# Optimization experiments

Hardware: AMD Instinct MI355X
Metric: run time of the kernel (lower is better)

The kernel has to match this reference:

```python
import jax, jax.numpy as jnp
import numpy as np


def setup_inputs() -> dict:
    key = jax.random.key(0)
    ks = jax.random.split(key, 8)
    B, D, H, W = 4, 96, 64, 64
    K, N, R = 4, 16, 6
    return {
        "x": jax.random.normal(ks[0], (B, D, H, W), jnp.float32),
        "x_proj_weight": jax.random.normal(ks[1], (K, R + 2 * N, D), jnp.float32) * 0.05,
        "dt_projs_weight": jax.random.normal(ks[2], (K, D, R), jnp.float32) * 0.1,
        "dt_projs_bias": jax.random.normal(ks[3], (K, D), jnp.float32) * 0.1,
        "A_logs": jax.random.uniform(ks[4], (K * D, N), jnp.float32),
        "Ds": jax.random.normal(ks[5], (K * D,), jnp.float32),
        "ln_weight": jnp.ones((D,), jnp.float32),
        "ln_bias": jnp.zeros((D,), jnp.float32),
    }


def reference(x, x_proj_weight, dt_projs_weight, dt_projs_bias, A_logs, Ds, ln_weight, ln_bias):
    B, D, H, W = x.shape
    K, _, R = dt_projs_weight.shape
    N = A_logs.shape[1]
    L = H * W

    # ---- CrossScan: 4 traversal orders (row-major, col-major, and their reverses) ----
    xf = x.reshape(B, D, L)                                   # row-major
    xt = jnp.transpose(x, (0, 1, 3, 2)).reshape(B, D, L)      # col-major
    xs = jnp.stack([xf, xt, xf[..., ::-1], xt[..., ::-1]], axis=1)  # (B, K, D, L)

    # ---- input-dependent projections ----
    x_dbl = jnp.einsum('bkdl,kcd->bkcl', xs, x_proj_weight)   # (B, K, R+2N, L)
    dts, Bs, Cs = jnp.split(x_dbl, [R, R + N], axis=2)        # Bs/Cs: (B, K, N, L)
    dts = jnp.einsum('bkrl,kdr->bkdl', dts, dt_projs_weight)  # (B, K, D, L)

    A = -jnp.exp(A_logs).reshape(K, D, N)                     # (K, D, N)
    delta = jax.nn.softplus(dts + dt_projs_bias[None, :, :, None])  # (B, K, D, L)

    # ---- selective (S6) scan over L ----
    def step(h, inp):
        d_t, u_t, B_t, C_t = inp  # (B,K,D) (B,K,D) (B,K,N) (B,K,N)
        dA = jnp.exp(d_t[..., None] * A[None])                # (B,K,D,N)
        h = h * dA + (d_t * u_t)[..., None] * B_t[:, :, None, :]
        y_t = jnp.einsum('bkdn,bkn->bkd', h, C_t)
        return h, y_t

    h0 = jnp.zeros((B, K, D, N), x.dtype)
    seq = (jnp.moveaxis(delta, -1, 0), jnp.moveaxis(xs, -1, 0),
           jnp.moveaxis(Bs, -1, 0), jnp.moveaxis(Cs, -1, 0))
    _, ys = jax.lax.scan(step, h0, seq)                       # (L, B, K, D)
    ys = jnp.moveaxis(ys, 0, -1)                              # (B, K, D, L)
    ys = ys + Ds.reshape(K, D)[None, :, :, None] * xs         # skip term D*u

    # ---- CrossMerge: undo the 4 traversal orders and sum ----
    m = ys[:, 0:2] + ys[:, 2:4][..., ::-1]                    # (B, 2, D, L)
    y = m[:, 0] + jnp.transpose(m[:, 1].reshape(B, D, W, H), (0, 1, 3, 2)).reshape(B, D, L)

    # ---- out_norm (LayerNorm over channels, v0 path) ----
    y = jnp.transpose(y, (0, 2, 1))                           # (B, L, D)
    mu = y.mean(-1, keepdims=True)
    var = y.var(-1, keepdims=True)
    y = (y - mu) / jnp.sqrt(var + 1e-5) * ln_weight + ln_bias
    return y.reshape(B, H, W, D)
```

## Files before the change

### kernel.cpp

```cpp
#include <hip/hip_runtime.h>
#include <math.h>

#define B_ 4
#define D_ 96
#define H_ 64
#define W_ 64
#define L_ 4096
#define K_ 4
#define N_ 16
#define R_ 6
#define C_ 38
#define SSX 128
#define CLSX (L_ / SSX)
#define CH_ (B_ * K_ * D_ * N_)

#if defined(__has_builtin)
#if __has_builtin(__builtin_amdgcn_exp2f)
#define EXP2F(x) __builtin_amdgcn_exp2f(x)
#else
#define EXP2F(x) exp2f(x)
#endif
#else
#define EXP2F(x) exp2f(x)
#endif
#define LOG2E 1.44269504f

__device__ __forceinline__ int src_idx(int k, int l) {
    int m = (k >= 2) ? (L_ - 1 - l) : l;
    if (k & 1) return ((m & 63) << 6) | (m >> 6);
    return m;
}

__device__ __forceinline__ float softplus_f(float a) {
    return (a > 15.f) ? a : __logf(1.f + __expf(a));
}

__global__ __launch_bounds__(256) void transpose_kernel(
    const float* __restrict__ x,
    float* __restrict__ xs2)
{
    int bid = blockIdx.x;
    int b = bid / (3 * 64);
    int rest = bid % (3 * 64);
    int dblk = rest / 64, lblk = rest % 64;
    int d0 = dblk * 32;
    int l0 = lblk * 64;
    int tid = threadIdx.x;

    __shared__ float s_t[32][65];

    for (int i = tid; i < 32 * 64; i += 256) {
        int d = i >> 6, l = i & 63;
        s_t[d][l] = x[((long)b * D_ + d0 + d) * L_ + l0 + l];
    }
    __syncthreads();

    for (int i = tid; i < 64 * 32; i += 256) {
        int l = i >> 5, d = i & 31;
        float v = s_t[d][l];
        xs2[((long)b * L_ + l0 + l) * D_ + d0 + d] = v;
        xs2[((long)(B_ + b) * L_ + l * 64 + lblk) * D_ + d0 + d] = v;
    }
}

__global__ __launch_bounds__(256) void proj_kernel(
    const float* __restrict__ xs2,
    const float* __restrict__ xpw,
    const float* __restrict__ wdt,
    const float* __restrict__ bdt,
    float* __restrict__ delta,
    float* __restrict__ Bsb,
    float* __restrict__ Csb)
{
    const int TL = 64;
    const int tiles = L_ / TL;
    int bid = blockIdx.x;
    int bk = bid / tiles;
    int tile = bid % tiles;
    int b = bk / K_, k = bk % K_;
    int l0 = tile * TL;
    int tid = threadIdx.x;

    __shared__ __align__(16) float s_wpT[D_ * 40];
    __shared__ __align__(16) float s_xs[D_ * 68];
    __shared__ __align__(16) float s_wdt[R_ * D_];
    __shared__ __align__(16) float s_bias[D_];
    __shared__ __align__(16) float s_dts[R_ * 68];

    for (int i = tid; i < C_ * D_; i += 256) {
        int d = i / C_, c = i % C_;
        int cp = (c < 6) ? c : c + 2;
        s_wpT[d * 40 + cp] = xpw[(k * C_ + c) * D_ + d];
    }
    for (int i = tid; i < 96; i += 256) {
        s_wpT[i * 40 + 6] = 0.f;
        s_wpT[i * 40 + 7] = 0.f;
    }
    for (int i = tid; i < R_ * D_; i += 256) {
        int r = i / D_, d = i % D_;
        s_wdt[i] = wdt[(k * D_ + d) * R_ + r];
    }
    if (tid < D_) s_bias[tid] = bdt[k * D_ + tid];

    const float* xsp = xs2 + (long)((k & 1) * B_ + b) * L_ * D_;
    for (int i = tid; i < TL * 24; i += 256) {
        int lt = i / 24, dq = i % 24;
        int row = (k < 2) ? (l0 + lt) : (L_ - 1 - l0 - lt);
        float4 v = *(const float4*)(xsp + (long)row * D_ + dq * 4);
        s_xs[(dq * 4 + 0) * 68 + lt] = v.x;
        s_xs[(dq * 4 + 1) * 68 + lt] = v.y;
        s_xs[(dq * 4 + 2) * 68 + lt] = v.z;
        s_xs[(dq * 4 + 3) * 68 + lt] = v.w;
    }
    __syncthreads();

    long base = (long)bk * L_ + l0;

    int ct = tid >> 4;
    int lt4 = (tid & 15) * 4;
    if (ct < 10) {
        int cp0 = ct * 4;
        float acc[4][4];
#pragma unroll
        for (int i = 0; i < 4; ++i)
#pragma unroll
            for (int j = 0; j < 4; ++j) acc[i][j] = 0.f;
#pragma unroll 4
        for (int d = 0; d < D_; ++d) {
            float4 wv = *(const float4*)(&s_wpT[d * 40 + cp0]);
            float4 xv = *(const float4*)(&s_xs[d * 68 + lt4]);
            float wa[4] = {wv.x, wv.y, wv.z, wv.w};
            float xa[4] = {xv.x, xv.y, xv.z, xv.w};
#pragma unroll
            for (int ci = 0; ci < 4; ++ci)
#pragma unroll
                for (int li = 0; li < 4; ++li)
                    acc[ci][li] += wa[ci] * xa[li];
        }
        if (ct == 0) {
#pragma unroll
            for (int ci = 0; ci < 4; ++ci)
                *(float4*)(&s_dts[ci * 68 + lt4]) =
                    make_float4(acc[ci][0], acc[ci][1], acc[ci][2], acc[ci][3]);
        } else if (ct == 1) {
#pragma unroll
            for (int ci = 0; ci < 2; ++ci)
                *(float4*)(&s_dts[(4 + ci) * 68 + lt4]) =
                    make_float4(acc[ci][0], acc[ci][1], acc[ci][2], acc[ci][3]);
        } else if (ct < 6) {
            int n0 = cp0 - 8;
#pragma unroll
            for (int li = 0; li < 4; ++li)
                *(float4*)(&Bsb[(base + lt4 + li) * N_ + n0]) =
                    make_float4(acc[0][li], acc[1][li], acc[2][li], acc[3][li]);
        } else {
            int n0 = cp0 - 24;
#pragma unroll
            for (int li = 0; li < 4; ++li)
                *(float4*)(&Csb[(base + lt4 + li) * N_ + n0]) =
                    make_float4(acc[0][li], acc[1][li], acc[2][li], acc[3][li]);
        }
    }
    __syncthreads();

    for (int tt = tid; tt < 24 * 16; tt += 256) {
        int dt = tt % 24, lt4b = (tt / 24) * 4;
        int d0 = dt * 4;
        float4 bias = *(const float4*)(&s_bias[d0]);
        float acc[4][4];
#pragma unroll
        for (int li = 0; li < 4; ++li) {
            acc[li][0] = bias.x; acc[li][1] = bias.y;
            acc[li][2] = bias.z; acc[li][3] = bias.w;
        }
#pragma unroll
        for (int r = 0; r < R_; ++r) {
            float4 wv = *(const float4*)(&s_wdt[r * D_ + d0]);
            float4 tv = *(const float4*)(&s_dts[r * 68 + lt4b]);
            float wa[4] = {wv.x, wv.y, wv.z, wv.w};
            float ta[4] = {tv.x, tv.y, tv.z, tv.w};
#pragma unroll
            for (int li = 0; li < 4; ++li)
#pragma unroll
                for (int di = 0; di < 4; ++di)
                    acc[li][di] += ta[li] * wa[di];
        }
#pragma unroll
        for (int li = 0; li < 4; ++li) {
            float4 o = make_float4(softplus_f(acc[li][0]), softplus_f(acc[li][1]),
                                   softplus_f(acc[li][2]), softplus_f(acc[li][3]));
            *(float4*)(&delta[(base + lt4b + li) * D_ + d0]) = o;
        }
    }
}

__global__ __launch_bounds__(384) void scan_part1(
    const float* __restrict__ A_logs,
    const float* __restrict__ xs2,
    const float* __restrict__ delta,
    const float* __restrict__ Bsb,
    float* __restrict__ pAarr,
    float* __restrict__ hharr)
{
    int tid = threadIdx.x;
    int sub = tid / 192;
    int r = tid % 192;
    int dd = r >> 1;
    int half = r & 1;
    int n0 = half * 8;
    int cid = blockIdx.x * 2 + sub;
    int bk = cid / SSX;
    int j = cid % SSX;
    int b = bk / K_, k = bk % K_;
    int kd = k * D_ + dd;
    int l0 = j * CLSX;

    float A2[8];
    {
        const float4* ap = (const float4*)(A_logs + kd * N_ + n0);
        float4 a0 = ap[0], a1 = ap[1];
        A2[0] = -__expf(a0.x) * LOG2E; A2[1] = -__expf(a0.y) * LOG2E;
        A2[2] = -__expf(a0.z) * LOG2E; A2[3] = -__expf(a0.w) * LOG2E;
        A2[4] = -__expf(a1.x) * LOG2E; A2[5] = -__expf(a1.y) * LOG2E;
        A2[6] = -__expf(a1.z) * LOG2E; A2[7] = -__expf(a1.w) * LOG2E;
    }

    const float* dp = delta + ((long)bk * L_ + l0) * D_ + dd;
    const float* bp = Bsb + ((long)bk * L_ + l0) * N_ + n0;
    const float* xsp = xs2 + (long)((k & 1) * B_ + b) * L_ * D_;
    long urow0 = (k < 2) ? l0 : (L_ - 1 - l0);
    long ustep = (k < 2) ? D_ : -D_;
    const float* up = xsp + urow0 * D_ + dd;

    float h[8];
#pragma unroll
    for (int i = 0; i < 8; ++i) h[i] = 0.f;
    float sdel = 0.f;

#pragma unroll 4
    for (int t = 0; t < CLSX; ++t) {
        float del = dp[(long)t * D_];
        float u   = up[(long)t * ustep];
        float4 b0 = *(const float4*)(bp + t * N_);
        float4 b1 = *(const float4*)(bp + t * N_ + 4);
        float Bv[8] = {b0.x, b0.y, b0.z, b0.w, b1.x, b1.y, b1.z, b1.w};
        sdel += del;
        float delu = del * u;
#pragma unroll
        for (int i = 0; i < 8; ++i) {
            float dA = EXP2F(del * A2[i]);
            h[i] = h[i] * dA + delu * Bv[i];
        }
    }

    long sbase = (long)j * CH_ + (long)(bk * D_ + dd) * N_ + n0;
    *(float4*)(pAarr + sbase) =
        make_float4(EXP2F(A2[0] * sdel), EXP2F(A2[1] * sdel),
                    EXP2F(A2[2] * sdel), EXP2F(A2[3] * sdel));
    *(float4*)(pAarr + sbase + 4) =
        make_float4(EXP2F(A2[4] * sdel), EXP2F(A2[5] * sdel),
                    EXP2F(A2[6] * sdel), EXP2F(A2[7] * sdel));
    *(float4*)(hharr + sbase)     = make_float4(h[0], h[1], h[2], h[3]);
    *(float4*)(hharr + sbase + 4) = make_float4(h[4], h[5], h[6], h[7]);
}

__global__ __launch_bounds__(256) void scan_combine(
    const float* __restrict__ pAarr,
    float* __restrict__ hharr)
{
    int c = blockIdx.x * 256 + threadIdx.x;
    float h = 0.f;
#pragma unroll 8
    for (int j = 0; j < SSX; ++j) {
        long idx = (long)j * CH_ + c;
        float tmp = hharr[idx];
        float pa  = pAarr[idx];
        hharr[idx] = h;
        h = tmp + pa * h;
    }
}

__global__ __launch_bounds__(384) void scan_part2_pair(
    const float* __restrict__ A_logs,
    const float* __restrict__ Ds,
    const float* __restrict__ xs2,
    const float* __restrict__ delta,
    const float* __restrict__ Bsb,
    const float* __restrict__ Csb,
    const float* __restrict__ hharr,
    float* __restrict__ ypair)
{
    __shared__ float s_y[2][CLSX][D_];

    int bid = blockIdx.x;
    int b = bid / (2 * SSX);
    int rest = bid % (2 * SSX);
    int p = rest / SSX;
    int j = rest % SSX;
    int tid = threadIdx.x;
    int g = tid / 192;
    int r = tid % 192;
    int dd = r >> 1;
    int half = r & 1;
    int n0 = half * 8;

    int kdir = p + 2 * g;
    int bk = b * K_ + kdir;
    int jj = g ? (SSX - 1 - j) : j;
    int l0s = jj * CLSX;
    int kd = kdir * D_ + dd;

    float A2[8];
    {
        const float4* ap = (const float4*)(A_logs + kd * N_ + n0);
        float4 a0 = ap[0], a1 = ap[1];
        A2[0] = -__expf(a0.x) * LOG2E; A2[1] = -__expf(a0.y) * LOG2E;
        A2[2] = -__expf(a0.z) * LOG2E; A2[3] = -__expf(a0.w) * LOG2E;
        A2[4] = -__expf(a1.x) * LOG2E; A2[5] = -__expf(a1.y) * LOG2E;
        A2[6] = -__expf(a1.z) * LOG2E; A2[7] = -__expf(a1.w) * LOG2E;
    }
    float Dv = Ds[kd];

    const float* dp = delta + ((long)bk * L_ + l0s) * D_ + dd;
    const float* bp = Bsb + ((long)bk * L_ + l0s) * N_ + n0;
    const float* cp = Csb + ((long)bk * L_ + l0s) * N_ + n0;
    const float* xsp = xs2 + (long)(p * B_ + b) * L_ * D_;
    long urow0 = g ? ((long)j * CLSX + CLSX - 1) : (long)l0s;
    long ustep = g ? -D_ : D_;
    const float* up = xsp + urow0 * D_ + dd;

    float h[8];
    {
        long sbase = (long)jj * CH_ + (long)(bk * D_ + dd) * N_ + n0;
        float4 h0 = *(const float4*)(hharr + sbase);
        float4 h1 = *(const float4*)(hharr + sbase + 4);
        h[0] = h0.x; h[1] = h0.y; h[2] = h0.z; h[3] = h0.w;
        h[4] = h1.x; h[5] = h1.y; h[6] = h1.z; h[7] = h1.w;
    }

#pragma unroll 4
    for (int t = 0; t < CLSX; ++t) {
        float del = dp[(long)t * D_];
        float u   = up[(long)t * ustep];
        float4 b0 = *(const float4*)(bp + t * N_);
        float4 b1 = *(const float4*)(bp + t * N_ + 4);
        float4 c0 = *(const float4*)(cp + t * N_);
        float4 c1 = *(const float4*)(cp + t * N_ + 4);
        float Bv[8] = {b0.x, b0.y, b0.z, b0.w, b1.x, b1.y, b1.z, b1.w};
        float Cv[8] = {c0.x, c0.y, c0.z, c0.w, c1.x, c1.y, c1.z, c1.w};
        float delu = del * u;
        float yv = 0.f;
#pragma unroll
        for (int i = 0; i < 8; ++i) {
            float dA = EXP2F(del * A2[i]);
            h[i] = h[i] * dA + delu * Bv[i];
            yv += h[i] * Cv[i];
        }
        yv += __shfl_xor(yv, 1);
        if (half == 0) {
            int tpos = g ? (CLSX - 1 - t) : t;
            s_y[g][tpos][dd] = yv + Dv * u;
        }
    }
    __syncthreads();

    float* yo = ypair + ((long)(p * B_ + b) * L_ + (long)j * CLSX) * D_;
    for (int i = tid; i < CLSX * 24; i += 384) {
        int lt = i / 24, dq = i % 24;
        int d0 = dq * 4;
        float4 o = make_float4(s_y[0][lt][d0 + 0] + s_y[1][lt][d0 + 0],
                               s_y[0][lt][d0 + 1] + s_y[1][lt][d0 + 1],
                               s_y[0][lt][d0 + 2] + s_y[1][lt][d0 + 2],
                               s_y[0][lt][d0 + 3] + s_y[1][lt][d0 + 3]);
        *(float4*)(yo + (long)lt * D_ + d0) = o;
    }
}

__global__ __launch_bounds__(256) void ln_merge_kernel(
    const float* __restrict__ ypair,
    const float* __restrict__ lnw,
    const float* __restrict__ lnb,
    float* __restrict__ out)
{
    int wid = (blockIdx.x * 256 + threadIdx.x) >> 6;
    int lane = threadIdx.x & 63;
    int b = wid / L_;
    int m = wid % L_;
    int mt = ((m & 63) << 6) | (m >> 6);

    const float* y0 = ypair + ((long)b * L_ + m) * D_;
    const float* y1 = ypair + ((long)(B_ + b) * L_ + mt) * D_;

    float v0 = y0[lane] + y1[lane];
    float v1 = (lane < 32) ? (y0[64 + lane] + y1[64 + lane]) : 0.f;

    float s  = v0 + v1;
    float s2 = v0 * v0 + v1 * v1;
#pragma unroll
    for (int mm = 1; mm < 64; mm <<= 1) {
        s  += __shfl_xor(s, mm);
        s2 += __shfl_xor(s2, mm);
    }
    float mu  = s * (1.f / D_);
    float var = s2 * (1.f / D_) - mu * mu;
    float rstd = rsqrtf(var + 1e-5f);

    long obase = (long)wid * D_;
    out[obase + lane] = (v0 - mu) * rstd * lnw[lane] + lnb[lane];
    if (lane < 32)
        out[obase + 64 + lane] = (v1 - mu) * rstd * lnw[64 + lane] + lnb[64 + lane];
}

__global__ __launch_bounds__(256) void proj_legacy(
    const float* __restrict__ x,
    const float* __restrict__ xpw,
    const float* __restrict__ wdt,
    const float* __restrict__ bdt,
    float* __restrict__ delta,
    float* __restrict__ Bsb,
    float* __restrict__ Csb)
{
    const int TL = 64;
    const int tiles = L_ / TL;
    int bid = blockIdx.x;
    int bk = bid / tiles;
    int tile = bid % tiles;
    int b = bk / K_, k = bk % K_;
    int l0 = tile * TL;
    int tid = threadIdx.x;

    __shared__ float s_wp[C_ * D_];
    __shared__ float s_wdt[R_ * D_];
    __shared__ float s_bias[D_];
    __shared__ float s_xs[D_ * (TL + 1)];
    __shared__ float s_xdbl[C_ * (TL + 1)];

    for (int i = tid; i < C_ * D_; i += 256) s_wp[i] = xpw[k * C_ * D_ + i];
    for (int i = tid; i < R_ * D_; i += 256) {
        int r = i / D_, d = i % D_;
        s_wdt[i] = wdt[(k * D_ + d) * R_ + r];
    }
    if (tid < D_) s_bias[tid] = bdt[k * D_ + tid];
    for (int i = tid; i < D_ * TL; i += 256) {
        int d = i / TL, lt = i % TL;
        s_xs[d * (TL + 1) + lt] = x[(b * D_ + d) * L_ + src_idx(k, l0 + lt)];
    }
    __syncthreads();

    for (int idx = tid; idx < C_ * TL; idx += 256) {
        int c = idx / TL, lt = idx % TL;
        const float* wr = &s_wp[c * D_];
        float acc = 0.f;
#pragma unroll 8
        for (int d = 0; d < D_; ++d) acc += wr[d] * s_xs[d * (TL + 1) + lt];
        s_xdbl[c * (TL + 1) + lt] = acc;
    }
    __syncthreads();

    long base = (long)bk * L_ + l0;
    for (int idx = tid; idx < TL * D_; idx += 256) {
        int lt = idx / D_, d = idx % D_;
        float acc = s_bias[d];
#pragma unroll
        for (int r = 0; r < R_; ++r)
            acc += s_wdt[r * D_ + d] * s_xdbl[r * (TL + 1) + lt];
        delta[(base + lt) * D_ + d] = softplus_f(acc);
    }
    for (int idx = tid; idx < TL * 2 * N_; idx += 256) {
        int lt = idx / (2 * N_), c2 = idx % (2 * N_);
        float v = s_xdbl[(R_ + c2) * (TL + 1) + lt];
        if (c2 < N_) Bsb[(base + lt) * N_ + c2] = v;
        else         Csb[(base + lt) * N_ + (c2 - N_)] = v;
    }
}

__global__ __launch_bounds__(64) void scan_serial(
    const float* __restrict__ x,
    const float* __restrict__ A_logs,
    const float* __restrict__ Ds,
    const float* __restrict__ delta,
    const float* __restrict__ Bsb,
    const float* __restrict__ Csb,
    float* __restrict__ ys)
{
    const int chans = D_ / 4;
    int bid = blockIdx.x;
    int bk = bid / chans;
    int d0 = (bid % chans) * 4;
    int b = bk / K_, k = bk % K_;
    int lane = threadIdx.x;
    int g = lane >> 4, n = lane & 15;
    int d = d0 + g;
    int kd = k * D_ + d;

    float A  = -__expf(A_logs[kd * N_ + n]);
    float Dv = Ds[kd];
    const float* dptr = delta + ((long)bk * L_) * D_ + d;
    const float* bptr = Bsb + (long)bk * L_ * N_ + n;
    const float* cptr = Csb + (long)bk * L_ * N_ + n;
    const float* xptr = x + ((long)b * D_ + d) * L_;
    float* yptr = ys + ((long)bk * L_) * D_ + d;

    float h = 0.f;
#pragma unroll 4
    for (int l = 0; l < L_; ++l) {
        float del = dptr[(long)l * D_];
        float u   = xptr[src_idx(k, l)];
        float Bt  = bptr[l * N_];
        float Ct  = cptr[l * N_];
        float dA  = __expf(del * A);
        h = h * dA + del * u * Bt;
        float yv = h * Ct;
        yv += __shfl_xor(yv, 1);
        yv += __shfl_xor(yv, 2);
        yv += __shfl_xor(yv, 4);
        yv += __shfl_xor(yv, 8);
        if (n == 0) yptr[(long)l * D_] = yv + Dv * u;
    }
}

__global__ __launch_bounds__(256) void merge_ln_kernel(
    const float* __restrict__ ys,
    const float* __restrict__ lnw,
    const float* __restrict__ lnb,
    float* __restrict__ out)
{
    int wid = (blockIdx.x * 256 + threadIdx.x) >> 6;
    int lane = threadIdx.x & 63;
    int b = wid / L_;
    int l = wid % L_;
    int lt = ((l & 63) << 6) | (l >> 6);

    long base0 = ((long)(b * K_ + 0) * L_ + l) * D_;
    long base2 = ((long)(b * K_ + 2) * L_ + (L_ - 1 - l)) * D_;
    long base1 = ((long)(b * K_ + 1) * L_ + lt) * D_;
    long base3 = ((long)(b * K_ + 3) * L_ + (L_ - 1 - lt)) * D_;

    int dA = lane;
    int dB = lane + 64;
    float v0 = ys[base0 + dA] + ys[base2 + dA] + ys[base1 + dA] + ys[base3 + dA];
    float v1 = 0.f;
    if (dB < D_)
        v1 = ys[base0 + dB] + ys[base2 + dB] + ys[base1 + dB] + ys[base3 + dB];

    float s  = v0 + v1;
    float s2 = v0 * v0 + v1 * v1;
#pragma unroll
    for (int m = 1; m < 64; m <<= 1) {
        s  += __shfl_xor(s, m);
        s2 += __shfl_xor(s2, m);
    }
    float mu  = s * (1.f / D_);
    float var = s2 * (1.f / D_) - mu * mu;
    float rstd = rsqrtf(var + 1e-5f);

    long obase = ((long)b * L_ + l) * D_;
    out[obase + dA] = (v0 - mu) * rstd * lnw[dA] + lnb[dA];
    if (dB < D_)
        out[obase + dB] = (v1 - mu) * rstd * lnw[dB] + lnb[dB];
}

extern "C" void kernel_launch(void* const* d_in, const int* in_sizes, int n_in,
                              void* d_out, int out_size, void* d_ws, size_t ws_size,
                              hipStream_t stream) {
    const float* x      = (const float*)d_in[0];
    const float* xpw    = (const float*)d_in[1];
    const float* wdt    = (const float*)d_in[2];
    const float* bdt    = (const float*)d_in[3];
    const float* A_logs = (const float*)d_in[4];
    const float* Ds     = (const float*)d_in[5];
    const float* lnw    = (const float*)d_in[6];
    const float* lnb    = (const float*)d_in[7];
    float* out = (float*)d_out;

    float* ws = (float*)d_ws;
    const long n_delta = (long)B_ * K_ * L_ * D_;
    const long n_bc    = (long)B_ * K_ * L_ * N_;
    const long n_bld   = (long)B_ * L_ * D_;
    const long n_sum   = (long)SSX * CH_;

    float* delta = ws;
    float* Bsb   = delta + n_delta;
    float* Csb   = Bsb + n_bc;
    float* xs2   = Csb + n_bc;
    float* ypair = xs2 + 2 * n_bld;
    float* hharr = ypair + 2 * n_bld;
    float* pAarr = ypair;
    size_t need = (size_t)(n_delta + 2 * n_bc + 4 * n_bld + n_sum) * 4;

    if (ws_size >= need) {
        transpose_kernel<<<B_ * 3 * 64, 256, 0, stream>>>(x, xs2);
        proj_kernel<<<B_ * K_ * (L_ / 64), 256, 0, stream>>>(
            xs2, xpw, wdt, bdt, delta, Bsb, Csb);
        scan_part1<<<B_ * K_ * SSX / 2, 384, 0, stream>>>(
            A_logs, xs2, delta, Bsb, pAarr, hharr);
        scan_combine<<<CH_ / 256, 256, 0, stream>>>(pAarr, hharr);
        scan_part2_pair<<<B_ * 2 * SSX, 384, 0, stream>>>(
            A_logs, Ds, xs2, delta, Bsb, Csb, hharr, ypair);
        ln_merge_kernel<<<(B_ * L_) / 4, 256, 0, stream>>>(ypair, lnw, lnb, out);
    } else {
        float* ys2 = Csb + n_bc;
        proj_legacy<<<B_ * K_ * (L_ / 64), 256, 0, stream>>>(
            x, xpw, wdt, bdt, delta, Bsb, Csb);
        scan_serial<<<B_ * K_ * (D_ / 4), 64, 0, stream>>>(
            x, A_logs, Ds, delta, Bsb, Csb, ys2);
        merge_ln_kernel<<<(B_ * L_) / 4, 256, 0, stream>>>(ys2, lnw, lnb, out);
    }
}
```

Before: 186.4 us.

## Fuse chunk-local scan pass into projection kernel using shared-memory tiles

Merges scan_part1 into the projection kernel, so each 64-position tile computes its two 32-step chunk partial states right after the projection. Delta is recomputed from the shared dt tile, and u and B are read from shared memory instead of global memory, which removes a kernel launch and a global re-read of delta, B and xs. In exchange, only 192 of 256 threads run the scan, each handling 16 states serially, which adds register pressure and lowers parallelism for this phase compared with the old 8-state split.

```diff
diff --git a/kernel.cpp b/kernel.cpp
--- a/kernel.cpp
+++ b/kernel.cpp
@@ -63,14 +63,17 @@
     }
 }
 
-__global__ __launch_bounds__(256) void proj_kernel(
+__global__ __launch_bounds__(256) void proj_scan_kernel(
     const float* __restrict__ xs2,
     const float* __restrict__ xpw,
     const float* __restrict__ wdt,
     const float* __restrict__ bdt,
+    const float* __restrict__ A_logs,
     float* __restrict__ delta,
     float* __restrict__ Bsb,
-    float* __restrict__ Csb)
+    float* __restrict__ Csb,
+    float* __restrict__ pAarr,
+    float* __restrict__ hharr)
 {
     const int TL = 64;
     const int tiles = L_ / TL;
@@ -86,6 +89,7 @@
     __shared__ __align__(16) float s_wdt[R_ * D_];
     __shared__ __align__(16) float s_bias[D_];
     __shared__ __align__(16) float s_dts[R_ * 68];
+    __shared__ __align__(16) float s_B[TL * N_];
 
     for (int i = tid; i < C_ * D_; i += 256) {
         int d = i / C_, c = i % C_;
@@ -150,9 +154,11 @@
         } else if (ct < 6) {
             int n0 = cp0 - 8;
 #pragma unroll
-            for (int li = 0; li < 4; ++li)
-                *(float4*)(&Bsb[(base + lt4 + li) * N_ + n0]) =
-                    make_float4(acc[0][li], acc[1][li], acc[2][li], acc[3][li]);
+            for (int li = 0; li < 4; ++li) {
+                float4 v = make_float4(acc[0][li], acc[1][li], acc[2][li], acc[3][li]);
+                *(float4*)(&Bsb[(base + lt4 + li) * N_ + n0]) = v;
+                *(float4*)(&s_B[(lt4 + li) * N_ + n0]) = v;
+            }
         } else {
             int n0 = cp0 - 24;
 #pragma unroll
@@ -192,76 +198,67 @@
             *(float4*)(&delta[(base + lt4b + li) * D_ + d0]) = o;
         }
     }
-}
-
-__global__ __launch_bounds__(384) void scan_part1(
-    const float* __restrict__ A_logs,
-    const float* __restrict__ xs2,
-    const float* __restrict__ delta,
-    const float* __restrict__ Bsb,
-    float* __restrict__ pAarr,
-    float* __restrict__ hharr)
-{
-    int tid = threadIdx.x;
-    int sub = tid / 192;
-    int r = tid % 192;
-    int dd = r >> 1;
-    int half = r & 1;
-    int n0 = half * 8;
-    int cid = blockIdx.x * 2 + sub;
-    int bk = cid / SSX;
-    int j = cid % SSX;
-    int b = bk / K_, k = bk % K_;
-    int kd = k * D_ + dd;
-    int l0 = j * CLSX;
-
-    float A2[8];
-    {
-        const float4* ap = (const float4*)(A_logs + kd * N_ + n0);
-        float4 a0 = ap[0], a1 = ap[1];
-        A2[0] = -__expf(a0.x) * LOG2E; A2[1] = -__expf(a0.y) * LOG2E;
-        A2[2] = -__expf(a0.z) * LOG2E; A2[3] = -__expf(a0.w) * LOG2E;
-        A2[4] = -__expf(a1.x) * LOG2E; A2[5] = -__expf(a1.y) * LOG2E;
-        A2[6] = -__expf(a1.z) * LOG2E; A2[7] = -__expf(a1.w) * LOG2E;
-    }
-
-    const float* dp = delta + ((long)bk * L_ + l0) * D_ + dd;
-    const float* bp = Bsb + ((long)bk * L_ + l0) * N_ + n0;
-    const float* xsp = xs2 + (long)((k & 1) * B_ + b) * L_ * D_;
-    long urow0 = (k < 2) ? l0 : (L_ - 1 - l0);
-    long ustep = (k < 2) ? D_ : -D_;
-    const float* up = xsp + urow0 * D_ + dd;
-
-    float h[8];
-#pragma unroll
-    for (int i = 0; i < 8; ++i) h[i] = 0.f;
-    float sdel = 0.f;
+
+    if (tid < 192) {
+        int sub = tid / 96;
+        int dd = tid % 96;
+        int j = tile * 2 + sub;
+        int kd = k * D_ + dd;
+
+        float A2[16];
+        {
+            const float4* ap = (const float4*)(A_logs + kd * N_);
+#pragma unroll
+            for (int q = 0; q < 4; ++q) {
+                float4 a = ap[q];
+                A2[q * 4 + 0] = -__expf(a.x) * LOG2E;
+                A2[q * 4 + 1] = -__expf(a.y) * LOG2E;
+                A2[q * 4 + 2] = -__expf(a.z) * LOG2E;
+                A2[q * 4 + 3] = -__expf(a.w) * LOG2E;
+            }
+        }
+        float wdtr[R_];
+#pragma unroll
+        for (int r = 0; r < R_; ++r) wdtr[r] = s_wdt[r * D_ + dd];
+        float biasv = s_bias[dd];
+
+        float h[16];
+#pragma unroll
+        for (int i = 0; i < 16; ++i) h[i] = 0.f;
+        float sdel = 0.f;
 
 #pragma unroll 4
-    for (int t = 0; t < CLSX; ++t) {
-        float del = dp[(long)t * D_];
-        float u   = up[(long)t * ustep];
-        float4 b0 = *(const float4*)(bp + t * N_);
-        float4 b1 = *(const float4*)(bp + t * N_ + 4);
-        float Bv[8] = {b0.x, b0.y, b0.z, b0.w, b1.x, b1.y, b1.z, b1.w};
-        sdel += del;
-        float delu = del * u;
-#pragma unroll
-        for (int i = 0; i < 8; ++i) {
-            float dA = EXP2F(del * A2[i]);
-            h[i] = h[i] * dA + delu * Bv[i];
-        }
-    }
-
-    long sbase = (long)j * CH_ + (long)(bk * D_ + dd) * N_ + n0;
-    *(float4*)(pAarr + sbase) =
-        make_float4(EXP2F(A2[0] * sdel), EXP2F(A2[1] * sdel),
-                    EXP2F(A2[2] * sdel), EXP2F(A2[3] * sdel));
-    *(float4*)(pAarr + sbase + 4) =
-        make_float4(EXP2F(A2[4] * sdel), EXP2F(A2[5] * sdel),
-                    EXP2F(A2[6] * sdel), EXP2F(A2[7] * sdel));
-    *(float4*)(hharr + sbase)     = make_float4(h[0], h[1], h[2], h[3]);
-    *(float4*)(hharr + sbase + 4) = make_float4(h[4], h[5], h[6], h[7]);
+        for (int t = 0; t < CLSX; ++t) {
+            int lt = sub * CLSX + t;
+            float acc = biasv;
+#pragma unroll
+            for (int r = 0; r < R_; ++r) acc += wdtr[r] * s_dts[r * 68 + lt];
+            float del = softplus_f(acc);
+            float u = s_xs[dd * 68 + lt];
+            float Bv[16];
+            *(float4*)(Bv + 0)  = *(const float4*)(&s_B[lt * N_ + 0]);
+            *(float4*)(Bv + 4)  = *(const float4*)(&s_B[lt * N_ + 4]);
+            *(float4*)(Bv + 8)  = *(const float4*)(&s_B[lt * N_ + 8]);
+            *(float4*)(Bv + 12) = *(const float4*)(&s_B[lt * N_ + 12]);
+            sdel += del;
+            float delu = del * u;
+#pragma unroll
+            for (int i = 0; i < 16; ++i) {
+                float dA = EXP2F(del * A2[i]);
+                h[i] = h[i] * dA + delu * Bv[i];
+            }
+        }
+
+        long sbase = (long)j * CH_ + (long)(bk * D_ + dd) * N_;
+#pragma unroll
+        for (int q = 0; q < 4; ++q) {
+            *(float4*)(pAarr + sbase + q * 4) =
+                make_float4(EXP2F(A2[q * 4 + 0] * sdel), EXP2F(A2[q * 4 + 1] * sdel),
+                            EXP2F(A2[q * 4 + 2] * sdel), EXP2F(A2[q * 4 + 3] * sdel));
+            *(float4*)(hharr + sbase + q * 4) =
+                make_float4(h[q * 4], h[q * 4 + 1], h[q * 4 + 2], h[q * 4 + 3]);
+        }
+    }
 }
 
 __global__ __launch_bounds__(256) void scan_combine(
@@ -590,10 +587,8 @@
 
     if (ws_size >= need) {
         transpose_kernel<<<B_ * 3 * 64, 256, 0, stream>>>(x, xs2);
-        proj_kernel<<<B_ * K_ * (L_ / 64), 256, 0, stream>>>(
-            xs2, xpw, wdt, bdt, delta, Bsb, Csb);
-        scan_part1<<<B_ * K_ * SSX / 2, 384, 0, stream>>>(
-            A_logs, xs2, delta, Bsb, pAarr, hharr);
+        proj_scan_kernel<<<B_ * K_ * (L_ / 64), 256, 0, stream>>>(
+            xs2, xpw, wdt, bdt, A_logs, delta, Bsb, Csb, pAarr, hharr);
         scan_combine<<<CH_ / 256, 256, 0, stream>>>(pAarr, hharr);
         scan_part2_pair<<<B_ * 2 * SSX, 384, 0, stream>>>(
             A_logs, Ds, xs2, delta, Bsb, Csb, hharr, ypair);
```

After: 182.6 us. 1.02x faster.
